# Performance work log

Measured on AMD Instinct MI355X. Metric: run time of the kernel, lower is better.

## Reference

```python
import jax, jax.numpy as jnp
import numpy as np

N_BINS = 15


def setup_inputs() -> dict:
    key = jax.random.key(0)
    k1, k2 = jax.random.split(key)
    N, C = 500000, 100
    logits = jax.random.normal(k1, (N, C), dtype=jnp.float32)
    labels = jax.random.randint(k2, (N,), 0, C, dtype=jnp.int64)
    return {"logits": logits, "labels": labels}


def _classwise_ece(logits, labels, n_bins=N_BINS):
    # Fused equivalent of the per-class, per-bin double loop.
    # Bins are (lower, upper] with boundaries linspace(0,1,n_bins+1),
    # so bin index = ceil(p * n_bins) - 1; p == 0 falls in NO bin.
    probs = jax.nn.softmax(logits, axis=1)            # [N, C]
    N, C = probs.shape
    valid = probs > 0.0                               # p==0 matched by no (lower, upper] bin
    bin_idx = jnp.clip(jnp.ceil(probs * n_bins).astype(jnp.int32) - 1, 0, n_bins - 1)

    class_ids = jnp.arange(C, dtype=jnp.int32)[None, :]          # [1, C]
    key = (jnp.broadcast_to(class_ids * n_bins, probs.shape) + bin_idx).reshape(-1)  # [N*C]

    w = valid.astype(probs.dtype)
    correct = (labels[:, None] == class_ids).astype(probs.dtype)  # labels_in_class

    num_seg = C * n_bins
    count = jax.ops.segment_sum(w.reshape(-1), key, num_segments=num_seg).reshape(C, n_bins)
    conf_sum = jax.ops.segment_sum((probs * w).reshape(-1), key, num_segments=num_seg).reshape(C, n_bins)
    acc_sum = jax.ops.segment_sum((correct * w).reshape(-1), key, num_segments=num_seg).reshape(C, n_bins)

    # |avg_conf - acc| * prop_in_bin == |conf_sum - acc_sum| / N; empty bins give 0.
    per_class_sce = jnp.sum(jnp.abs(conf_sum - acc_sum), axis=1) / N   # [C]
    sce = jnp.mean(per_class_sce)
    return sce, per_class_sce


def reference(logits, labels):
    return _classwise_ece(logits, labels)
```

## Files before the change

### kernel.cpp

```cpp
#include <hip/hip_runtime.h>
#include <math.h>

#define NCLS 100
#define NBINS 15
#define NSEG (NCLS * NBINS)
#define RPI 8

__device__ __forceinline__ void fadd(float* p, float v) { unsafeAtomicAdd(p, v); }

template <int CTRL>
__device__ __forceinline__ float dpp_add(float x) {
    int y = __builtin_amdgcn_update_dpp(0, __builtin_bit_cast(int, x),
                                        CTRL, 0xf, 0xf, true);
    return x + __builtin_bit_cast(float, y);
}

__global__ __launch_bounds__(256) void ece_main_kernel(
    const float* __restrict__ logits,
    const int* __restrict__ labels,
    float* __restrict__ g_total,
    float* __restrict__ g_conf,
    float* __restrict__ g_acc,
    int N)
{
    __shared__ float s_total[NCLS];
    __shared__ float s_conf[NSEG];
    __shared__ float s_acc[NSEG];
    for (int i = threadIdx.x; i < NSEG; i += 256) { s_conf[i] = 0.f; s_acc[i] = 0.f; }
    if (threadIdx.x < NCLS) s_total[threadIdx.x] = 0.f;
    __syncthreads();

    const int lane   = threadIdx.x & 63;
    const int wave   = threadIdx.x >> 6;
    const int gwave  = blockIdx.x * 4 + wave;
    const int nwaves = gridDim.x * 4;

    const int c0 = lane;
    const int c1 = lane + 64;
    const bool has1 = (c1 < NCLS);

    float t0 = 0.f, t1 = 0.f;

    for (int base = gwave * RPI; base < N; base += nwaves * RPI) {
        const int labv = labels[min(base + lane, N - 1)];

        float e0[RPI], e1[RPI], s[RPI];

        #pragma unroll
        for (int r = 0; r < RPI; ++r) {
            const int row = base + r;
            const bool v = (row < N);
            const float* rp = logits + (size_t)row * NCLS;
            e0[r] = v ? rp[c0] : -1000.f;
            e1[r] = (v && has1) ? rp[c1] : -1000.f;
        }

        #pragma unroll
        for (int r = 0; r < RPI; ++r) {
            e0[r] = __expf(e0[r]);
            e1[r] = __expf(e1[r]);
            s[r] = e0[r] + e1[r];
        }

        #pragma unroll
        for (int r = 0; r < RPI; ++r) s[r] = dpp_add<0x111>(s[r]);
        #pragma unroll
        for (int r = 0; r < RPI; ++r) s[r] = dpp_add<0x112>(s[r]);
        #pragma unroll
        for (int r = 0; r < RPI; ++r) s[r] = dpp_add<0x114>(s[r]);
        #pragma unroll
        for (int r = 0; r < RPI; ++r) s[r] = dpp_add<0x118>(s[r]);
        #pragma unroll
        for (int r = 0; r < RPI; ++r) s[r] = dpp_add<0x142>(s[r]);
        #pragma unroll
        for (int r = 0; r < RPI; ++r) s[r] = dpp_add<0x143>(s[r]);

        #pragma unroll
        for (int r = 0; r < RPI; ++r) {
            const float tot = __builtin_bit_cast(float,
                __builtin_amdgcn_readlane(__builtin_bit_cast(int, s[r]), 63));
            const float inv = __builtin_amdgcn_rcpf(fmaxf(tot, 1e-30f));
            const int lab = (base + r < N)
                          ? __builtin_amdgcn_readlane(labv, r) : -1;

            const float p0 = e0[r] * inv;
            t0 += p0;
            int b0 = min((int)ceilf(p0 * 15.f) - 1, NBINS - 1);
            if (b0 >= 1) fadd(&s_conf[c0 * NBINS + b0], p0);
            if (c0 == lab) fadd(&s_acc[c0 * NBINS + max(b0, 0)], 1.f);

            const float p1 = e1[r] * inv;
            t1 += p1;
            int b1 = min((int)ceilf(p1 * 15.f) - 1, NBINS - 1);
            if (b1 >= 1) fadd(&s_conf[c1 * NBINS + b1], p1);
            if (has1 && c1 == lab) fadd(&s_acc[c1 * NBINS + max(b1, 0)], 1.f);
        }
    }

    fadd(&s_total[c0], t0);
    if (has1) fadd(&s_total[c1], t1);
    __syncthreads();

    for (int i = threadIdx.x; i < NSEG; i += 256) {
        float v = s_conf[i]; if (v != 0.f) fadd(&g_conf[i], v);
        float a = s_acc[i];  if (a != 0.f) fadd(&g_acc[i], a);
    }
    if (threadIdx.x < NCLS) {
        float t = s_total[threadIdx.x];
        if (t != 0.f) fadd(&g_total[threadIdx.x], t);
    }
}

__global__ __launch_bounds__(128) void ece_final_kernel(
    const float* __restrict__ g_total,
    const float* __restrict__ g_conf,
    const float* __restrict__ g_acc,
    float* __restrict__ out,
    float invN)
{
    __shared__ float red[128];
    const int t = threadIdx.x;
    float s = 0.f;
    if (t < NCLS) {
        float conf0 = g_total[t];
        float sum = 0.f;
        #pragma unroll
        for (int b = 1; b < NBINS; ++b) {
            float cb = g_conf[t * NBINS + b];
            float ab = g_acc[t * NBINS + b];
            conf0 -= cb;
            sum += fabsf(cb - ab);
        }
        sum += fabsf(conf0 - g_acc[t * NBINS + 0]);
        s = sum * invN;
        out[1 + t] = s;
    }
    red[t] = s;
    __syncthreads();
    #pragma unroll
    for (int off = 64; off > 0; off >>= 1) {
        if (t < off) red[t] += red[t + off];
        __syncthreads();
    }
    if (t == 0) out[0] = red[0] * (1.0f / (float)NCLS);
}

extern "C" void kernel_launch(void* const* d_in, const int* in_sizes, int n_in,
                              void* d_out, int out_size, void* d_ws, size_t ws_size,
                              hipStream_t stream)
{
    const float* logits = (const float*)d_in[0];
    const int*   labels = (const int*)d_in[1];
    const int N = in_sizes[1];
    float* out = (float*)d_out;

    float* g_total = (float*)d_ws;
    float* g_conf  = g_total + NCLS;
    float* g_acc   = g_conf + NSEG;

    (void)hipMemsetAsync(d_ws, 0, (size_t)(NCLS + 2 * NSEG) * sizeof(float), stream);

    const int blocks = 2048;
    ece_main_kernel<<<blocks, 256, 0, stream>>>(logits, labels,
                                                g_total, g_conf, g_acc, N);
    ece_final_kernel<<<1, 128, 0, stream>>>(g_total, g_conf, g_acc, out,
                                            1.0f / (float)N);
}
```

Measured before the change: 352.1 us.

## Vectorize logits loads with float2 and pad LDS bins, dropping total-based bin0 trick

New measurement: 847.0 us. 141% more time.

```diff
diff --git a/kernel.cpp b/kernel.cpp
--- a/kernel.cpp
+++ b/kernel.cpp
@@ -3,7 +3,7 @@
 
 #define NCLS 100
 #define NBINS 15
-#define NSEG (NCLS * NBINS)
+#define CELLS 1952
 #define RPI 8
 
 __device__ __forceinline__ void fadd(float* p, float v) { unsafeAtomicAdd(p, v); }
@@ -14,20 +14,21 @@
                                         CTRL, 0xf, 0xf, true);
     return x + __builtin_bit_cast(float, y);
 }
+__device__ __forceinline__ float rlf(float x, int l) {
+    return __builtin_bit_cast(float,
+        __builtin_amdgcn_readlane(__builtin_bit_cast(int, x), l));
+}
 
 __global__ __launch_bounds__(256) void ece_main_kernel(
     const float* __restrict__ logits,
     const int* __restrict__ labels,
-    float* __restrict__ g_total,
     float* __restrict__ g_conf,
     float* __restrict__ g_acc,
     int N)
 {
-    __shared__ float s_total[NCLS];
-    __shared__ float s_conf[NSEG];
-    __shared__ float s_acc[NSEG];
-    for (int i = threadIdx.x; i < NSEG; i += 256) { s_conf[i] = 0.f; s_acc[i] = 0.f; }
-    if (threadIdx.x < NCLS) s_total[threadIdx.x] = 0.f;
+    __shared__ float s_conf[CELLS];
+    __shared__ float s_acc[CELLS];
+    for (int i = threadIdx.x; i < CELLS; i += 256) { s_conf[i] = 0.f; s_acc[i] = 0.f; }
     __syncthreads();
 
     const int lane   = threadIdx.x & 63;
@@ -35,31 +36,24 @@
     const int gwave  = blockIdx.x * 4 + wave;
     const int nwaves = gridDim.x * 4;
 
-    const int c0 = lane;
-    const int c1 = lane + 64;
-    const bool has1 = (c1 < NCLS);
-
-    float t0 = 0.f, t1 = 0.f;
+    const int q    = lane * 2;
+    const bool act = (q < NCLS);
+    const int qoff = act ? q : 0;
+    const int cell0 = q * NBINS + (q >> 2);
+    const int cell1 = (q + 1) * NBINS + ((q + 1) >> 2);
 
     for (int base = gwave * RPI; base < N; base += nwaves * RPI) {
         const int labv = labels[min(base + lane, N - 1)];
 
         float e0[RPI], e1[RPI], s[RPI];
-
         #pragma unroll
         for (int r = 0; r < RPI; ++r) {
-            const int row = base + r;
-            const bool v = (row < N);
-            const float* rp = logits + (size_t)row * NCLS;
-            e0[r] = v ? rp[c0] : -1000.f;
-            e1[r] = (v && has1) ? rp[c1] : -1000.f;
-        }
-
-        #pragma unroll
-        for (int r = 0; r < RPI; ++r) {
-            e0[r] = __expf(e0[r]);
-            e1[r] = __expf(e1[r]);
-            s[r] = e0[r] + e1[r];
+            const int rowc = min(base + r, N - 1);
+            const bool v = act && (base + r < N);
+            const float2 x = *(const float2*)(logits + (size_t)rowc * NCLS + qoff);
+            e0[r] = __expf(v ? x.x : -1000.f);
+            e1[r] = __expf(v ? x.y : -1000.f);
+            s[r]  = e0[r] + e1[r];
         }
 
         #pragma unroll
@@ -77,42 +71,31 @@
 
         #pragma unroll
         for (int r = 0; r < RPI; ++r) {
-            const float tot = __builtin_bit_cast(float,
-                __builtin_amdgcn_readlane(__builtin_bit_cast(int, s[r]), 63));
+            const float tot = rlf(s[r], 63);
             const float inv = __builtin_amdgcn_rcpf(fmaxf(tot, 1e-30f));
-            const int lab = (base + r < N)
-                          ? __builtin_amdgcn_readlane(labv, r) : -1;
+            const int  lab  = __builtin_amdgcn_readlane(labv, r);
+            const bool rv   = (base + r < N);
 
             const float p0 = e0[r] * inv;
-            t0 += p0;
-            int b0 = min((int)ceilf(p0 * 15.f) - 1, NBINS - 1);
-            if (b0 >= 1) fadd(&s_conf[c0 * NBINS + b0], p0);
-            if (c0 == lab) fadd(&s_acc[c0 * NBINS + max(b0, 0)], 1.f);
+            int b0 = min(max((int)ceilf(p0 * 15.f) - 1, 0), NBINS - 1);
+            fadd(&s_conf[cell0 + b0], p0);
+            fadd(&s_acc [cell0 + b0], (rv && q == lab) ? 1.f : 0.f);
 
             const float p1 = e1[r] * inv;
-            t1 += p1;
-            int b1 = min((int)ceilf(p1 * 15.f) - 1, NBINS - 1);
-            if (b1 >= 1) fadd(&s_conf[c1 * NBINS + b1], p1);
-            if (has1 && c1 == lab) fadd(&s_acc[c1 * NBINS + max(b1, 0)], 1.f);
+            int b1 = min(max((int)ceilf(p1 * 15.f) - 1, 0), NBINS - 1);
+            fadd(&s_conf[cell1 + b1], p1);
+            fadd(&s_acc [cell1 + b1], (rv && (q + 1) == lab) ? 1.f : 0.f);
         }
     }
 
-    fadd(&s_total[c0], t0);
-    if (has1) fadd(&s_total[c1], t1);
     __syncthreads();
-
-    for (int i = threadIdx.x; i < NSEG; i += 256) {
-        float v = s_conf[i]; if (v != 0.f) fadd(&g_conf[i], v);
-        float a = s_acc[i];  if (a != 0.f) fadd(&g_acc[i], a);
-    }
-    if (threadIdx.x < NCLS) {
-        float t = s_total[threadIdx.x];
-        if (t != 0.f) fadd(&g_total[threadIdx.x], t);
+    for (int i = threadIdx.x; i < CELLS; i += 256) {
+        const float v = s_conf[i]; if (v != 0.f) fadd(&g_conf[i], v);
+        const float a = s_acc[i];  if (a != 0.f) fadd(&g_acc[i], a);
     }
 }
 
 __global__ __launch_bounds__(128) void ece_final_kernel(
-    const float* __restrict__ g_total,
     const float* __restrict__ g_conf,
     const float* __restrict__ g_acc,
     float* __restrict__ out,
@@ -122,16 +105,11 @@
     const int t = threadIdx.x;
     float s = 0.f;
     if (t < NCLS) {
-        float conf0 = g_total[t];
+        const int cb = t * NBINS + (t >> 2);
         float sum = 0.f;
         #pragma unroll
-        for (int b = 1; b < NBINS; ++b) {
-            float cb = g_conf[t * NBINS + b];
-            float ab = g_acc[t * NBINS + b];
-            conf0 -= cb;
-            sum += fabsf(cb - ab);
-        }
-        sum += fabsf(conf0 - g_acc[t * NBINS + 0]);
+        for (int b = 0; b < NBINS; ++b)
+            sum += fabsf(g_conf[cb + b] - g_acc[cb + b]);
         s = sum * invN;
         out[1 + t] = s;
     }
@@ -154,15 +132,12 @@
     const int N = in_sizes[1];
     float* out = (float*)d_out;
 
-    float* g_total = (float*)d_ws;
-    float* g_conf  = g_total + NCLS;
-    float* g_acc   = g_conf + NSEG;
+    float* g_conf = (float*)d_ws;
+    float* g_acc  = g_conf + CELLS;
 
-    (void)hipMemsetAsync(d_ws, 0, (size_t)(NCLS + 2 * NSEG) * sizeof(float), stream);
+    (void)hipMemsetAsync(d_ws, 0, (size_t)2 * CELLS * sizeof(float), stream);
 
     const int blocks = 2048;
-    ece_main_kernel<<<blocks, 256, 0, stream>>>(logits, labels,
-                                                g_total, g_conf, g_acc, N);
-    ece_final_kernel<<<1, 128, 0, stream>>>(g_total, g_conf, g_acc, out,
-                                            1.0f / (float)N);
+    ece_main_kernel<<<blocks, 256, 0, stream>>>(logits, labels, g_conf, g_acc, N);
+    ece_final_kernel<<<1, 128, 0, stream>>>(g_conf, g_acc, out, 1.0f / (float)N);
 }
```
